# Performance work log

Hardware: AMD Instinct MI355X
Metric: run time of the kernel (lower is better)

The kernel has to match this reference:

```python
import jax, jax.numpy as jnp
import numpy as np

B, P, D, V = 8192, 32, 128, 100000  # batch, max path len, embed dim, label_num


def setup_inputs() -> dict:
    key = jax.random.key(0)
    k1, k2, k3, k4, k5, k6 = jax.random.split(key, 6)
    return {
        "hidden_": jax.random.normal(k1, (B, D), dtype=jnp.float32),
        "target": jax.random.randint(k2, (B,), 0, V, dtype=jnp.int64),
        "target_path": jax.random.randint(k3, (B, P), 0, V, dtype=jnp.int64),
        "target_path_len": jax.random.randint(k4, (B,), 1, P, dtype=jnp.int64),
        "target_code": jax.random.randint(k5, (B, P), 0, 2, dtype=jnp.int64),
        "embed_table": jax.random.normal(k6, (V, D), dtype=jnp.float32) * 0.02,
    }


def reference(hidden_, target, target_path, target_path_len, target_code, embed_table):
    # embeds: [B, P, D] gather of tree-node vectors along each label's path
    embeds = embed_table[target_path]
    # per-node score: sigmoid(<node_vec, hidden>) -> [B, P]
    score = jax.nn.sigmoid(jnp.einsum("bpd,bd->bp", embeds, hidden_))
    flag = target_code.astype(jnp.float32)
    # BCE-style per-node loss, exactly as the TF code writes it
    loss = -jnp.log(flag * score + (1.0 - flag) * (1.0 - score))
    # ragged path mask: positions < target_path_len are valid (tf.ragged.range + batch_gather)
    mask = (jnp.arange(P)[None, :] < target_path_len[:, None]).astype(jnp.float32)
    # reduce_mean over the ragged tensor = sum of valid losses / total valid count
    return jnp.sum(loss * mask) / jnp.sum(mask)
```

## Files before the change

kernel.cpp:

```cpp
#include <hip/hip_runtime.h>

#define BB 8192
#define PP 32
#define DD 128

__global__ __launch_bounds__(256) void hs_loss_kernel(
    const float* __restrict__ hidden,
    const int*   __restrict__ path,
    const int*   __restrict__ path_len,
    const int*   __restrict__ code,
    const float* __restrict__ embed,
    float2* __restrict__ partials)
{
    const int tid = threadIdx.x;
    const int w   = tid >> 6;
    const int l   = tid & 63;
    const int h   = l >> 5;
    const int hl  = l & 31;
    const int b   = blockIdx.x * 4 + w;

    __shared__ float plds[4][PP * 33];
    float* const myp = plds[w];

    const int len   = path_len[b];
    const int idx_l = path[b * PP + hl];
    const int cd_l  = code[b * PP + hl];

    const float4 hv = ((const float4*)(hidden + (size_t)b * DD))[hl];

    #pragma unroll
    for (int batch = 0; batch < 4; ++batch) {
        const int p0 = batch * 8;
        if (p0 < len) {
            int pid[4];
            float4 e[4];
            #pragma unroll
            for (int j = 0; j < 4; ++j) {
                pid[j] = p0 + 2 * j + h;
                const int idx = __shfl(idx_l, pid[j]);
                if (pid[j] < len)
                    e[j] = ((const float4*)(embed + (size_t)idx * DD))[hl];
            }
            #pragma unroll
            for (int j = 0; j < 4; ++j) {
                if (pid[j] < len) {
                    const float pr = e[j].x * hv.x + e[j].y * hv.y
                                   + e[j].z * hv.z + e[j].w * hv.w;
                    myp[pid[j] * 33 + hl] = pr;
                }
            }
        }
    }

    const int lp = l & 31;
    const int kb = h * 16;
    float psum = 0.0f;
    #pragma unroll
    for (int k = 0; k < 16; ++k) psum += myp[lp * 33 + kb + k];
    const float dot = psum + __shfl_xor(psum, 32);

    float loss = 0.0f;
    if (l < 32 && lp < len) {
        const float z = cd_l ? -dot : dot;
        loss = fmaxf(z, 0.0f) + __logf(1.0f + __expf(-fabsf(z)));
    }
    #pragma unroll
    for (int m = 1; m <= 32; m <<= 1) loss += __shfl_xor(loss, m);
    if (l == 0) partials[b] = make_float2(loss, (float)len);
}

__global__ __launch_bounds__(1024) void hs_finalize_kernel(
    const float2* __restrict__ partials, float* __restrict__ out)
{
    const int tid = threadIdx.x;
    float ls = 0.0f, cs = 0.0f;
    #pragma unroll
    for (int k = 0; k < BB / 1024; ++k) {
        const float2 v = partials[tid + k * 1024];
        ls += v.x;
        cs += v.y;
    }
    #pragma unroll
    for (int m = 1; m <= 32; m <<= 1) {
        ls += __shfl_xor(ls, m);
        cs += __shfl_xor(cs, m);
    }
    __shared__ float s_l[16], s_c[16];
    const int wave = tid >> 6;
    if ((tid & 63) == 0) { s_l[wave] = ls; s_c[wave] = cs; }
    __syncthreads();
    if (tid == 0) {
        float L = 0.0f, C = 0.0f;
        #pragma unroll
        for (int wv = 0; wv < 16; ++wv) { L += s_l[wv]; C += s_c[wv]; }
        out[0] = L / C;
    }
}

extern "C" void kernel_launch(void* const* d_in, const int* in_sizes, int n_in,
                              void* d_out, int out_size, void* d_ws, size_t ws_size,
                              hipStream_t stream) {
    const float* hidden   = (const float*)d_in[0];
    const int*   path     = (const int*)d_in[2];
    const int*   path_len = (const int*)d_in[3];
    const int*   code     = (const int*)d_in[4];
    const float* embed    = (const float*)d_in[5];
    float*  out      = (float*)d_out;
    float2* partials = (float2*)d_ws;

    hs_loss_kernel<<<BB / 4, 256, 0, stream>>>(hidden, path, path_len, code,
                                               embed, partials);
    hs_finalize_kernel<<<1, 1024, 0, stream>>>(partials, out);
}
```

Before: 100.5 us.

## Split each batch row's path across two waves to double parallelism

Each batch row is now handled by two wavefronts, each covering 16 of the 32 path positions, with an early exit when a half has no valid positions. The launch has twice as many blocks and the finalize kernel reduces twice as many partials. The aim is more memory-level parallelism in the embedding gathers and shorter per-wave dependency chains. The cost is that hidden, path and code are loaded twice per row, and the reduction does extra shuffles.

```diff
diff --git a/kernel.cpp b/kernel.cpp
--- a/kernel.cpp
+++ b/kernel.cpp
@@ -3,6 +3,7 @@
 #define BB 8192
 #define PP 32
 #define DD 128
+#define HP 16
 
 __global__ __launch_bounds__(256) void hs_loss_kernel(
     const float* __restrict__ hidden,
@@ -17,56 +18,68 @@
     const int l   = tid & 63;
     const int h   = l >> 5;
     const int hl  = l & 31;
-    const int b   = blockIdx.x * 4 + w;
+    const int gw  = blockIdx.x * 4 + w;
+    const int b   = gw >> 1;
+    const int s   = (gw & 1) << 4;
 
-    __shared__ float plds[4][PP * 33];
+    __shared__ float plds[4][HP * 33];
     float* const myp = plds[w];
 
-    const int len   = path_len[b];
+    const int len     = path_len[b];
+    const int len_loc = min(max(len - s, 0), HP);
+
+    if (len_loc == 0) {
+        if (l == 0) partials[gw] = make_float2(0.0f, 0.0f);
+        return;
+    }
+
     const int idx_l = path[b * PP + hl];
     const int cd_l  = code[b * PP + hl];
 
     const float4 hv = ((const float4*)(hidden + (size_t)b * DD))[hl];
 
     #pragma unroll
-    for (int batch = 0; batch < 4; ++batch) {
+    for (int batch = 0; batch < 2; ++batch) {
         const int p0 = batch * 8;
-        if (p0 < len) {
-            int pid[4];
+        if (p0 < len_loc) {
+            int pl[4];
             float4 e[4];
             #pragma unroll
             for (int j = 0; j < 4; ++j) {
-                pid[j] = p0 + 2 * j + h;
-                const int idx = __shfl(idx_l, pid[j]);
-                if (pid[j] < len)
+                pl[j] = p0 + 2 * j + h;
+                const int idx = __shfl(idx_l, s + pl[j]);
+                if (pl[j] < len_loc)
                     e[j] = ((const float4*)(embed + (size_t)idx * DD))[hl];
             }
             #pragma unroll
             for (int j = 0; j < 4; ++j) {
-                if (pid[j] < len) {
+                if (pl[j] < len_loc) {
                     const float pr = e[j].x * hv.x + e[j].y * hv.y
                                    + e[j].z * hv.z + e[j].w * hv.w;
-                    myp[pid[j] * 33 + hl] = pr;
+                    myp[pl[j] * 33 + hl] = pr;
                 }
             }
         }
     }
 
-    const int lp = l & 31;
-    const int kb = h * 16;
+    const int lp = l & 15;
+    const int kb = (l >> 4) * 8;
     float psum = 0.0f;
     #pragma unroll
-    for (int k = 0; k < 16; ++k) psum += myp[lp * 33 + kb + k];
-    const float dot = psum + __shfl_xor(psum, 32);
+    for (int k = 0; k < 8; ++k) psum += myp[lp * 33 + kb + k];
+    float dot = psum + __shfl_xor(psum, 16);
+    dot += __shfl_xor(dot, 32);
+
+    const int cd = __shfl(cd_l, s + lp);
 
     float loss = 0.0f;
-    if (l < 32 && lp < len) {
-        const float z = cd_l ? -dot : dot;
+    if (l < 16 && lp < len_loc) {
+        const float z = cd ? -dot : dot;
         loss = fmaxf(z, 0.0f) + __logf(1.0f + __expf(-fabsf(z)));
     }
     #pragma unroll
-    for (int m = 1; m <= 32; m <<= 1) loss += __shfl_xor(loss, m);
-    if (l == 0) partials[b] = make_float2(loss, (float)len);
+    for (int m = 1; m <= 8; m <<= 1) loss += __shfl_xor(loss, m);
+    if (l == 0) partials[gw] = make_float2(loss, (float)len_loc);
 }
 
 __global__ __launch_bounds__(1024) void hs_finalize_kernel(
@@ -75,7 +88,7 @@
     const int tid = threadIdx.x;
     float ls = 0.0f, cs = 0.0f;
     #pragma unroll
-    for (int k = 0; k < BB / 1024; ++k) {
+    for (int k = 0; k < (2 * BB) / 1024; ++k) {
         const float2 v = partials[tid + k * 1024];
         ls += v.x;
         cs += v.y;
@@ -108,7 +121,7 @@
     float*  out      = (float*)d_out;
     float2* partials = (float2*)d_ws;
 
-    hs_loss_kernel<<<BB / 4, 256, 0, stream>>>(hidden, path, path_len, code,
-                                               embed, partials);
+    hs_loss_kernel<<<(2 * BB) / 4, 256, 0, stream>>>(hidden, path, path_len,
+                                                     code, embed, partials);
     hs_finalize_kernel<<<1, 1024, 0, stream>>>(partials, out);
 }
```

Result: no change. 102.1 us (+1.6%).
